# Kernel optimization log

Measured on AMD Instinct MI355X. Metric: run time of the kernel, lower is better.

The kernel has to match this reference:

```python
import jax, jax.numpy as jnp
import numpy as np

N_GRAPHS = 1000  # fixed num_segments (torch uses batch.max()+1; ids drawn in [0, N_GRAPHS))


def setup_inputs() -> dict:
    key = jax.random.key(0)
    ks = jax.random.split(key, 12)
    n, d, h, e = 100000, 128, 128, 1600000
    x = jax.random.normal(ks[0], (n, d), jnp.float32)
    edge_index = jax.random.randint(ks[1], (2, e), 0, n)
    batch = jnp.sort(jax.random.randint(ks[2], (n,), 0, N_GRAPHS))

    def lin_w(k, i, o):
        return jax.random.normal(k, (i, o), jnp.float32) / np.sqrt(i).astype(np.float32)

    return {
        "x": x, "edge_index": edge_index, "batch": batch,
        "W0": lin_w(ks[3], d, h), "b0": jnp.zeros((h,), jnp.float32),
        "W1": lin_w(ks[4], h, h), "b1": jnp.zeros((h,), jnp.float32),
        "W2": lin_w(ks[5], h, h), "b2": jnp.zeros((h,), jnp.float32),
        "Wp1": lin_w(ks[6], h, h), "bp1": jnp.zeros((h,), jnp.float32),
        "Wp2": lin_w(ks[7], h, 1), "bp2": jnp.zeros((1,), jnp.float32),
    }


def reference(x, edge_index, batch, W0, b0, W1, b1, W2, b2, Wp1, bp1, Wp2, bp2):
    n = x.shape[0]
    src, dst = edge_index[0], edge_index[1]
    loop = jnp.arange(n, dtype=edge_index.dtype)
    src_a = jnp.concatenate([src, loop])  # [E+N]
    dst_a = jnp.concatenate([dst, loop])  # [E+N]

    # degree with self-loops, symmetric GCN norm per edge
    deg = jax.ops.segment_sum(jnp.ones_like(dst_a, dtype=x.dtype), dst_a, num_segments=n)
    dd = deg[src_a] * deg[dst_a]
    norm = jnp.where(dd > 0, jax.lax.rsqrt(dd), jnp.zeros_like(dd))  # [E+N]

    for W, b in ((W0, b0), (W1, b1), (W2, b2)):
        h = x @ W + b                              # [N, H] dense linear
        msg = h[src_a] * norm[:, None]             # gather + scale, [E+N, H]
        out = jax.ops.segment_sum(msg, dst_a, num_segments=n)  # scatter-add
        x = jax.nn.relu(out)

    # segment-mean pool over graphs
    pool = jax.ops.segment_sum(x, batch, num_segments=N_GRAPHS)  # [G, H]
    cnt = jax.ops.segment_sum(jnp.ones((n,), x.dtype), batch, num_segments=N_GRAPHS)
    pool = pool / jnp.clip(cnt, 1.0)[:, None]

    hid = jax.nn.relu(pool @ Wp1 + bp1)
    return (hid @ Wp2 + bp2).squeeze(-1)  # [G]
```

## Files before the change

### kernel.cpp

```cpp
#include <hip/hip_runtime.h>
#include <hip/hip_bf16.h>
#include <math.h>


typedef float f32x4 __attribute__((ext_vector_type(4)));
typedef short s16x8 __attribute__((ext_vector_type(8)));
typedef _Float16 f16;
typedef _Float16 f16x4 __attribute__((ext_vector_type(4)));

__device__ __forceinline__ unsigned short f2bf(float x) {
  unsigned u = __float_as_uint(x);
  unsigned r = (u + 0x7FFFu + ((u >> 16) & 1u)) >> 16;
  return (unsigned short)r;
}

__device__ __forceinline__ void wsplit_body(
    int blk, const float* __restrict__ W0, const float* __restrict__ W1,
    const float* __restrict__ W2, short* __restrict__ Whi, short* __restrict__ Wlo) {
  int layer = blk >> 6;
  int i = (blk & 63) * 256 + threadIdx.x;
  const float* W = (layer == 0) ? W0 : (layer == 1) ? W1 : W2;
  int j = i & 7, lane = (i >> 3) & 63, ks = (i >> 9) & 3, nt = i >> 11;
  int k = ks * 32 + (lane >> 4) * 8 + j;
  int nn = nt * 16 + (lane & 15);
  float w = W[k * 128 + nn];
  unsigned short h = f2bf(w);
  float hf = __uint_as_float(((unsigned)h) << 16);
  Whi[layer * 16384 + i] = (short)h;
  Wlo[layer * 16384 + i] = (short)f2bf(w - hf);
}

__global__ __launch_bounds__(256) void uber0_kernel(
    const int* __restrict__ src, const int* __restrict__ dst,
    int* __restrict__ cnt, int* __restrict__ bucket, int E,
    const float* __restrict__ W0, const float* __restrict__ W1,
    const float* __restrict__ W2, short* __restrict__ Whi, short* __restrict__ Wlo,
    const int* __restrict__ batch, int* __restrict__ gptr, int n, int G,
    float* __restrict__ pool, int CD, int GBD) {
  int b = blockIdx.x;
  if (b < CD) {
    int e = b * 256 + threadIdx.x;
    if (e < E) {
      int s = src[e], d = dst[e];
      int r = atomicAdd(&cnt[d], 1);
      if (r < 64) bucket[(d << 6) + r] = s;
    }
  } else if (b < CD + 192) {
    wsplit_body(b - CD, W0, W1, W2, Whi, Wlo);
  } else if (b < CD + 192 + GBD) {
    int i = (b - CD - 192) * 256 + threadIdx.x;
    if (i < n) {
      int bb = batch[i];
      if (i == 0) {
        for (int g = 0; g <= bb; ++g) gptr[g] = 0;
      } else {
        int bp = batch[i - 1];
        for (int g = bp + 1; g <= bb; ++g) gptr[g] = i;
      }
      if (i == n - 1) {
        for (int g = bb + 1; g <= G; ++g) gptr[g] = n;
      }
    }
  } else {
    int i = (b - CD - 192 - GBD) * 256 + threadIdx.x;
    if (i * 4 < G * 128) ((float4*)pool)[i] = make_float4(0.f, 0.f, 0.f, 0.f);
  }
}

__global__ __launch_bounds__(256) void gemm1_kernel(
    const float* __restrict__ X, const short* __restrict__ Whi,
    const short* __restrict__ Wlo, const float* __restrict__ bias,
    const int* __restrict__ cnt, float* __restrict__ rsq,
    f16* __restrict__ H, int n) {
  int wave = threadIdx.x >> 6, lane = threadIdx.x & 63;
  int quad = lane >> 4, m = lane & 15;
  int mbase = blockIdx.x * 64 + wave * 16;
  int row = min(mbase + m, n - 1);
  const float* xr = X + (size_t)row * 128 + quad * 8;
  const s16x8* WH = (const s16x8*)Whi;
  const s16x8* WL = (const s16x8*)Wlo;
  f32x4 acc[8];
#pragma unroll
  for (int nt = 0; nt < 8; ++nt) acc[nt] = 0.f;
#pragma unroll
  for (int ks = 0; ks < 4; ++ks) {
    float4 xa = *(const float4*)(xr + ks * 32);
    float4 xb = *(const float4*)(xr + ks * 32 + 4);
    float xs[8] = {xa.x, xa.y, xa.z, xa.w, xb.x, xb.y, xb.z, xb.w};
    s16x8 ah, al;
#pragma unroll
    for (int j = 0; j < 8; ++j) {
      unsigned short h = f2bf(xs[j]);
      float hf = __uint_as_float(((unsigned)h) << 16);
      ah[j] = (short)h;
      al[j] = (short)f2bf(xs[j] - hf);
    }
#pragma unroll
    for (int nt = 0; nt < 8; ++nt) {
      s16x8 wh = WH[(nt * 4 + ks) * 64 + lane];
      s16x8 wl = WL[(nt * 4 + ks) * 64 + lane];
      acc[nt] = __builtin_amdgcn_mfma_f32_16x16x32_bf16(ah, wh, acc[nt], 0, 0, 0);
      acc[nt] = __builtin_amdgcn_mfma_f32_16x16x32_bf16(al, wh, acc[nt], 0, 0, 0);
      acc[nt] = __builtin_amdgcn_mfma_f32_16x16x32_bf16(ah, wl, acc[nt], 0, 0, 0);
    }
  }
  float rs[4];
#pragma unroll
  for (int r = 0; r < 4; ++r) {
    int rr = mbase + quad * 4 + r;
    rs[r] = (rr < n) ? (1.0f / sqrtf((float)(cnt[rr] + 1))) : 0.f;
  }
  if (m == 0) {
#pragma unroll
    for (int r = 0; r < 4; ++r) {
      int rr = mbase + quad * 4 + r;
      if (rr < n) rsq[rr] = rs[r];
    }
  }
#pragma unroll
  for (int nt = 0; nt < 8; ++nt) {
    int col = nt * 16 + m;
    float bb = bias[col];
#pragma unroll
    for (int r = 0; r < 4; ++r) {
      int rr = mbase + quad * 4 + r;
      if (rr < n) H[(size_t)rr * 128 + col] = (f16)((acc[nt][r] + bb) * rs[r]);
    }
  }
}

__device__ __forceinline__ f32x4 agg_sum(
    const f16* __restrict__ H, const int* __restrict__ cnt,
    const int* __restrict__ bucket, int node, int hl) {
  const char* Hb = (const char*)H;
  unsigned hoff = (unsigned)hl << 3;
  int beg = node << 6;
  int end = beg + min(cnt[node], 64);
  f32x4 a = __builtin_convertvector(
      *(const f16x4*)(Hb + (((unsigned)node << 8) | hoff)), f32x4);
#define ROW(s) (*(const f16x4*)(Hb + (((unsigned)(s) << 8) + hoff)))
  for (int base = beg; base < end; base += 32) {
    int m = end - base;
    if (m > 32) m = 32;
    int sl = (hl < m) ? bucket[base + hl] : 0;
    int j = 0;
    for (; j + 15 < m; j += 16) {
      int s0 = __shfl(sl, j + 0, 32), s1 = __shfl(sl, j + 1, 32);
      int s2 = __shfl(sl, j + 2, 32), s3 = __shfl(sl, j + 3, 32);
      int s4 = __shfl(sl, j + 4, 32), s5 = __shfl(sl, j + 5, 32);
      int s6 = __shfl(sl, j + 6, 32), s7 = __shfl(sl, j + 7, 32);
      int s8 = __shfl(sl, j + 8, 32), s9 = __shfl(sl, j + 9, 32);
      int sa = __shfl(sl, j + 10, 32), sb = __shfl(sl, j + 11, 32);
      int sc = __shfl(sl, j + 12, 32), sd = __shfl(sl, j + 13, 32);
      int se = __shfl(sl, j + 14, 32), sf = __shfl(sl, j + 15, 32);
      f16x4 h0 = ROW(s0), h1 = ROW(s1), h2 = ROW(s2), h3 = ROW(s3);
      f16x4 h4 = ROW(s4), h5 = ROW(s5), h6 = ROW(s6), h7 = ROW(s7);
      f16x4 h8 = ROW(s8), h9 = ROW(s9), ha = ROW(sa), hb = ROW(sb);
      f16x4 hc = ROW(sc), hd = ROW(sd), he = ROW(se), hf = ROW(sf);
      f16x4 t0 = ((h0 + h1) + (h2 + h3)) + ((h4 + h5) + (h6 + h7));
      f16x4 t1 = ((h8 + h9) + (ha + hb)) + ((hc + hd) + (he + hf));
      a += __builtin_convertvector(t0, f32x4);
      a += __builtin_convertvector(t1, f32x4);
    }
    for (; j + 7 < m; j += 8) {
      int s0 = __shfl(sl, j + 0, 32), s1 = __shfl(sl, j + 1, 32);
      int s2 = __shfl(sl, j + 2, 32), s3 = __shfl(sl, j + 3, 32);
      int s4 = __shfl(sl, j + 4, 32), s5 = __shfl(sl, j + 5, 32);
      int s6 = __shfl(sl, j + 6, 32), s7 = __shfl(sl, j + 7, 32);
      f16x4 h0 = ROW(s0), h1 = ROW(s1), h2 = ROW(s2), h3 = ROW(s3);
      f16x4 h4 = ROW(s4), h5 = ROW(s5), h6 = ROW(s6), h7 = ROW(s7);
      f16x4 t0 = ((h0 + h1) + (h2 + h3)) + ((h4 + h5) + (h6 + h7));
      a += __builtin_convertvector(t0, f32x4);
    }
    for (; j + 3 < m; j += 4) {
      int s0 = __shfl(sl, j + 0, 32), s1 = __shfl(sl, j + 1, 32);
      int s2 = __shfl(sl, j + 2, 32), s3 = __shfl(sl, j + 3, 32);
      f16x4 t0 = (ROW(s0) + ROW(s1)) + (ROW(s2) + ROW(s3));
      a += __builtin_convertvector(t0, f32x4);
    }
    for (; j < m; ++j) {
      int s0 = __shfl(sl, j, 32);
      a += __builtin_convertvector(ROW(s0), f32x4);
    }
  }
#undef ROW
  return a;
}

#define LDS_STRIDE 132
__global__ __launch_bounds__(256) void agg_gemm_kernel(
    const f16* __restrict__ H, const int* __restrict__ cnt,
    const int* __restrict__ bucket, const float* __restrict__ rsq,
    const short* __restrict__ Whi, const short* __restrict__ Wlo,
    const float* __restrict__ bias, f16* __restrict__ Hout, int n) {
  __shared__ int lds[16 * LDS_STRIDE];
  int hw = threadIdx.x >> 5, hl = threadIdx.x & 31;
  int nbase = blockIdx.x * 16;
#pragma unroll
  for (int rep = 0; rep < 2; ++rep) {
    int nl = hw + rep * 8;
    int node = nbase + nl;
    f32x4 o = 0.f;
    if (node < n) {
      f32x4 s = agg_sum(H, cnt, bucket, node, hl);
      float r = rsq[node];
      o.x = fmaxf(s.x * r, 0.f);
      o.y = fmaxf(s.y * r, 0.f);
      o.z = fmaxf(s.z * r, 0.f);
      o.w = fmaxf(s.w * r, 0.f);
    }
    int* dst = lds + nl * LDS_STRIDE + hl * 4;
#pragma unroll
    for (int c = 0; c < 4; ++c) {
      float v = o[c];
      unsigned short h = f2bf(v);
      float hf = __uint_as_float(((unsigned)h) << 16);
      unsigned short l = f2bf(v - hf);
      dst[c] = (int)((((unsigned)h) << 16) | l);
    }
  }
  __syncthreads();

  int wave = threadIdx.x >> 6, lane = threadIdx.x & 63;
  int quad = lane >> 4, m = lane & 15;
  const s16x8* WH = (const s16x8*)Whi;
  const s16x8* WL = (const s16x8*)Wlo;
  f32x4 acc0 = 0.f, acc1 = 0.f;
  int nt0 = wave * 2, nt1 = wave * 2 + 1;
#pragma unroll
  for (int ks = 0; ks < 4; ++ks) {
    const int* arow = lds + m * LDS_STRIDE + ks * 32 + quad * 8;
    s16x8 ah, al;
#pragma unroll
    for (int j = 0; j < 8; ++j) {
      unsigned p = (unsigned)arow[j];
      ah[j] = (short)(p >> 16);
      al[j] = (short)(p & 0xffffu);
    }
    s16x8 wh0 = WH[(nt0 * 4 + ks) * 64 + lane];
    s16x8 wl0 = WL[(nt0 * 4 + ks) * 64 + lane];
    s16x8 wh1 = WH[(nt1 * 4 + ks) * 64 + lane];
    s16x8 wl1 = WL[(nt1 * 4 + ks) * 64 + lane];
    acc0 = __builtin_amdgcn_mfma_f32_16x16x32_bf16(ah, wh0, acc0, 0, 0, 0);
    acc0 = __builtin_amdgcn_mfma_f32_16x16x32_bf16(al, wh0, acc0, 0, 0, 0);
    acc0 = __builtin_amdgcn_mfma_f32_16x16x32_bf16(ah, wl0, acc0, 0, 0, 0);
    acc1 = __builtin_amdgcn_mfma_f32_16x16x32_bf16(ah, wh1, acc1, 0, 0, 0);
    acc1 = __builtin_amdgcn_mfma_f32_16x16x32_bf16(al, wh1, acc1, 0, 0, 0);
    acc1 = __builtin_amdgcn_mfma_f32_16x16x32_bf16(ah, wl1, acc1, 0, 0, 0);
  }
  float rs[4];
#pragma unroll
  for (int r = 0; r < 4; ++r) {
    int rr = nbase + quad * 4 + r;
    rs[r] = (rr < n) ? rsq[rr] : 0.f;
  }
#pragma unroll
  for (int t = 0; t < 2; ++t) {
    int nt = wave * 2 + t;
    int col = nt * 16 + m;
    float b = bias[col];
    f32x4 a = t ? acc1 : acc0;
#pragma unroll
    for (int r = 0; r < 4; ++r) {
      int rr = nbase + quad * 4 + r;
      if (rr < n) Hout[(size_t)rr * 128 + col] = (f16)((a[r] + b) * rs[r]);
    }
  }
}

__global__ __launch_bounds__(256) void agg_pool_kernel(
    const f16* __restrict__ H, const int* __restrict__ cnt,
    const int* __restrict__ bucket, const float* __restrict__ rsq,
    const int* __restrict__ batch, float* __restrict__ pool, int n) {
  __shared__ float rows[16][128];
  __shared__ int gids[16];
  int hw = threadIdx.x >> 5, hl = threadIdx.x & 31;
  int nbase = blockIdx.x * 16;
#pragma unroll
  for (int rep = 0; rep < 2; ++rep) {
    int nl = hw + rep * 8;
    int node = nbase + nl;
    f32x4 o = 0.f;
    if (node < n) {
      f32x4 s = agg_sum(H, cnt, bucket, node, hl);
      float r = rsq[node];
      o.x = fmaxf(s.x * r, 0.f);
      o.y = fmaxf(s.y * r, 0.f);
      o.z = fmaxf(s.z * r, 0.f);
      o.w = fmaxf(s.w * r, 0.f);
    }
    *(f32x4*)&rows[nl][hl * 4] = o;
    if (hl == 0) gids[nl] = (node < n) ? batch[node] : -1;
  }
  __syncthreads();
  int half = threadIdx.x >> 7;
  int ch = threadIdx.x & 127;
  float acc = 0.f;
  int curg = gids[half * 8];
  for (int i = half * 8; i < half * 8 + 8; ++i) {
    int g = gids[i];
    if (g != curg) {
      if (curg >= 0) atomicAdd(&pool[(size_t)curg * 128 + ch], acc);
      acc = 0.f;
      curg = g;
    }
    if (g >= 0) acc += rows[i][ch];
  }
  if (curg >= 0) atomicAdd(&pool[(size_t)curg * 128 + ch], acc);
}

__global__ __launch_bounds__(128) void head_kernel(
    const float* __restrict__ pool, const int* __restrict__ gptr,
    const float* __restrict__ Wp1, const float* __restrict__ bp1,
    const float* __restrict__ Wp2, const float* __restrict__ bp2,
    float* __restrict__ out, int G) {
  int g = blockIdx.x;
  int j = threadIdx.x;
  __shared__ float ps[128];
  __shared__ float hs[128];
  int cnt = gptr[g + 1] - gptr[g];
  float inv = 1.0f / (float)max(cnt, 1);
  ps[j] = pool[(size_t)g * 128 + j] * inv;
  __syncthreads();
  float acc = bp1[j];
#pragma unroll 8
  for (int k = 0; k < 128; ++k) acc = fmaf(ps[k], Wp1[k * 128 + j], acc);
  hs[j] = fmaxf(acc, 0.f) * Wp2[j];
  __syncthreads();
  for (int off = 64; off > 0; off >>= 1) {
    if (j < off) hs[j] += hs[j + off];
    __syncthreads();
  }
  if (j == 0) out[g] = hs[0] + bp2[0];
}

extern "C" void kernel_launch(void* const* d_in, const int* in_sizes, int n_in,
                              void* d_out, int out_size, void* d_ws, size_t ws_size,
                              hipStream_t stream) {
  const float* x    = (const float*)d_in[0];
  const int*   eidx = (const int*)d_in[1];
  const int*   batch= (const int*)d_in[2];
  const float* W0 = (const float*)d_in[3];
  const float* b0 = (const float*)d_in[4];
  const float* W1 = (const float*)d_in[5];
  const float* b1 = (const float*)d_in[6];
  const float* W2 = (const float*)d_in[7];
  const float* b2 = (const float*)d_in[8];
  const float* Wp1 = (const float*)d_in[9];
  const float* bp1 = (const float*)d_in[10];
  const float* Wp2 = (const float*)d_in[11];
  const float* bp2 = (const float*)d_in[12];
  float* out = (float*)d_out;

  const int N = in_sizes[0] / 128;
  const int E = in_sizes[1] / 2;
  const int G = out_size;

  const int* src = eidx;
  const int* dst = eidx + E;

  char* ws = (char*)d_ws;
  size_t off = 0;
  auto alloc = [&](size_t bytes) -> void* {
    void* p = ws + off;
    off = (off + bytes + 255) & ~(size_t)255;
    return p;
  };
  int*   cnt     = (int*)  alloc((size_t)N * 4);
  int*   bucket  = (int*)  alloc((size_t)N * 64 * 4);
  float* rsq     = (float*)alloc((size_t)N * 4);
  f16*   bufA    = (f16*)  alloc((size_t)N * 128 * 2);
  f16*   bufB    = (f16*)  alloc((size_t)N * 128 * 2);
  int*   gptr    = (int*)  alloc((size_t)(G + 1) * 4);
  float* pool    = (float*)alloc((size_t)G * 128 * 4);
  short* whi     = (short*)alloc(3 * 16384 * 2);
  short* wlo     = (short*)alloc(3 * 16384 * 2);
  (void)ws_size;

  hipMemsetAsync(cnt, 0, (size_t)N * 4, stream);

  const int CD  = (E + 255) / 256;
  const int GBD = (N + 255) / 256;
  const int PZ  = (G * 128 / 4 + 255) / 256;
  uber0_kernel<<<CD + 192 + GBD + PZ, 256, 0, stream>>>(
      src, dst, cnt, bucket, E, W0, W1, W2, whi, wlo, batch, gptr, N, G, pool,
      CD, GBD);

  gemm1_kernel<<<(N + 63) / 64, 256, 0, stream>>>(
      x, whi, wlo, b0, cnt, rsq, bufA, N);

  dim3 fused_grid((N + 15) / 16);
  agg_gemm_kernel<<<fused_grid, 256, 0, stream>>>(bufA, cnt, bucket, rsq,
      whi + 16384, wlo + 16384, b1, bufB, N);
  agg_gemm_kernel<<<fused_grid, 256, 0, stream>>>(bufB, cnt, bucket, rsq,
      whi + 2 * 16384, wlo + 2 * 16384, b2, bufA, N);
  agg_pool_kernel<<<fused_grid, 256, 0, stream>>>(bufA, cnt, bucket, rsq, batch, pool, N);

  head_kernel<<<G, 128, 0, stream>>>(pool, gptr, Wp1, bp1, Wp2, bp2, out, G);
}
```

Baseline: 483.2 us.

## Tile feature buffers by channel group and split aggregation from GEMM

Stores layer activations as 8 column tiles of 16 fp16 channels each, contiguous per node. Aggregation is split into per-tile blocks so that the blockIdx&7 tile choice lines up with round-robin XCD dispatch, letting each XCD's L2 hold one roughly 3.2 MB tile during the random neighbour gathers. The fused agg+GEMM kernels are replaced by separate aggregation and full 128-wide GEMM kernels, which adds an intermediate buffer R that is written and read again. The edge bucket fill becomes a two-phase scheme: record per-edge ranks, then scatter with nontemporal stores inside the first GEMM launch. The degree normalization now clamps the neighbour count to 64.

```diff
diff --git a/kernel.cpp b/kernel.cpp
--- a/kernel.cpp
+++ b/kernel.cpp
@@ -7,6 +7,7 @@
 typedef short s16x8 __attribute__((ext_vector_type(8)));
 typedef _Float16 f16;
 typedef _Float16 f16x4 __attribute__((ext_vector_type(4)));
+typedef _Float16 f16x8 __attribute__((ext_vector_type(8)));
 
 __device__ __forceinline__ unsigned short f2bf(float x) {
   unsigned u = __float_as_uint(x);
@@ -31,8 +32,8 @@
 }
 
 __global__ __launch_bounds__(256) void uber0_kernel(
-    const int* __restrict__ src, const int* __restrict__ dst,
-    int* __restrict__ cnt, int* __restrict__ bucket, int E,
+    const int* __restrict__ dst, int* __restrict__ cnt, int* __restrict__ rank,
+    int E,
     const float* __restrict__ W0, const float* __restrict__ W1,
     const float* __restrict__ W2, short* __restrict__ Whi, short* __restrict__ Wlo,
     const int* __restrict__ batch, int* __restrict__ gptr, int n, int G,
@@ -41,9 +42,8 @@
   if (b < CD) {
     int e = b * 256 + threadIdx.x;
     if (e < E) {
-      int s = src[e], d = dst[e];
-      int r = atomicAdd(&cnt[d], 1);
-      if (r < 64) bucket[(d << 6) + r] = s;
+      int d = __builtin_nontemporal_load(dst + e);
+      rank[e] = atomicAdd(&cnt[d], 1);
     }
   } else if (b < CD + 192) {
     wsplit_body(b - CD, W0, W1, W2, Whi, Wlo);
@@ -67,14 +67,27 @@
   }
 }
 
-__global__ __launch_bounds__(256) void gemm1_kernel(
+__global__ __launch_bounds__(256) void fill_gemm1_kernel(
+    const int* __restrict__ src, const int* __restrict__ dstv,
+    const int* __restrict__ rank, int* __restrict__ bucket, int E, int FB,
     const float* __restrict__ X, const short* __restrict__ Whi,
     const short* __restrict__ Wlo, const float* __restrict__ bias,
-    const int* __restrict__ cnt, float* __restrict__ rsq,
-    f16* __restrict__ H, int n) {
+    const int* __restrict__ cnt, f16* __restrict__ H, int n) {
+  int b = blockIdx.x;
+  if (b < FB) {
+    int i = b * 256 + threadIdx.x;
+    if (i < E) {
+      int s = __builtin_nontemporal_load(src + i);
+      int d = __builtin_nontemporal_load(dstv + i);
+      int r = __builtin_nontemporal_load(rank + i);
+      if (r < 64)
+        __builtin_nontemporal_store(s, bucket + (((size_t)d) << 6) + r);
+    }
+    return;
+  }
   int wave = threadIdx.x >> 6, lane = threadIdx.x & 63;
   int quad = lane >> 4, m = lane & 15;
-  int mbase = blockIdx.x * 64 + wave * 16;
+  int mbase = (b - FB) * 64 + wave * 16;
   int row = min(mbase + m, n - 1);
   const float* xr = X + (size_t)row * 128 + quad * 8;
   const s16x8* WH = (const s16x8*)Whi;
@@ -108,14 +121,7 @@
 #pragma unroll
   for (int r = 0; r < 4; ++r) {
     int rr = mbase + quad * 4 + r;
-    rs[r] = (rr < n) ? (1.0f / sqrtf((float)(cnt[rr] + 1))) : 0.f;
-  }
-  if (m == 0) {
-#pragma unroll
-    for (int r = 0; r < 4; ++r) {
-      int rr = mbase + quad * 4 + r;
-      if (rr < n) rsq[rr] = rs[r];
-    }
+    rs[r] = (rr < n) ? (1.0f / sqrtf((float)(min(cnt[rr], 64) + 1))) : 0.f;
   }
 #pragma unroll
   for (int nt = 0; nt < 8; ++nt) {
@@ -124,189 +130,198 @@
 #pragma unroll
     for (int r = 0; r < 4; ++r) {
       int rr = mbase + quad * 4 + r;
-      if (rr < n) H[(size_t)rr * 128 + col] = (f16)((acc[nt][r] + bb) * rs[r]);
-    }
-  }
-}
-
-__device__ __forceinline__ f32x4 agg_sum(
-    const f16* __restrict__ H, const int* __restrict__ cnt,
-    const int* __restrict__ bucket, int node, int hl) {
-  const char* Hb = (const char*)H;
-  unsigned hoff = (unsigned)hl << 3;
-  int beg = node << 6;
-  int end = beg + min(cnt[node], 64);
-  f32x4 a = __builtin_convertvector(
-      *(const f16x4*)(Hb + (((unsigned)node << 8) | hoff)), f32x4);
-#define ROW(s) (*(const f16x4*)(Hb + (((unsigned)(s) << 8) + hoff)))
-  for (int base = beg; base < end; base += 32) {
-    int m = end - base;
-    if (m > 32) m = 32;
-    int sl = (hl < m) ? bucket[base + hl] : 0;
-    int j = 0;
-    for (; j + 15 < m; j += 16) {
-      int s0 = __shfl(sl, j + 0, 32), s1 = __shfl(sl, j + 1, 32);
-      int s2 = __shfl(sl, j + 2, 32), s3 = __shfl(sl, j + 3, 32);
-      int s4 = __shfl(sl, j + 4, 32), s5 = __shfl(sl, j + 5, 32);
-      int s6 = __shfl(sl, j + 6, 32), s7 = __shfl(sl, j + 7, 32);
-      int s8 = __shfl(sl, j + 8, 32), s9 = __shfl(sl, j + 9, 32);
-      int sa = __shfl(sl, j + 10, 32), sb = __shfl(sl, j + 11, 32);
-      int sc = __shfl(sl, j + 12, 32), sd = __shfl(sl, j + 13, 32);
-      int se = __shfl(sl, j + 14, 32), sf = __shfl(sl, j + 15, 32);
-      f16x4 h0 = ROW(s0), h1 = ROW(s1), h2 = ROW(s2), h3 = ROW(s3);
-      f16x4 h4 = ROW(s4), h5 = ROW(s5), h6 = ROW(s6), h7 = ROW(s7);
-      f16x4 h8 = ROW(s8), h9 = ROW(s9), ha = ROW(sa), hb = ROW(sb);
-      f16x4 hc = ROW(sc), hd = ROW(sd), he = ROW(se), hf = ROW(sf);
-      f16x4 t0 = ((h0 + h1) + (h2 + h3)) + ((h4 + h5) + (h6 + h7));
-      f16x4 t1 = ((h8 + h9) + (ha + hb)) + ((hc + hd) + (he + hf));
-      a += __builtin_convertvector(t0, f32x4);
-      a += __builtin_convertvector(t1, f32x4);
-    }
-    for (; j + 7 < m; j += 8) {
-      int s0 = __shfl(sl, j + 0, 32), s1 = __shfl(sl, j + 1, 32);
-      int s2 = __shfl(sl, j + 2, 32), s3 = __shfl(sl, j + 3, 32);
-      int s4 = __shfl(sl, j + 4, 32), s5 = __shfl(sl, j + 5, 32);
-      int s6 = __shfl(sl, j + 6, 32), s7 = __shfl(sl, j + 7, 32);
-      f16x4 h0 = ROW(s0), h1 = ROW(s1), h2 = ROW(s2), h3 = ROW(s3);
-      f16x4 h4 = ROW(s4), h5 = ROW(s5), h6 = ROW(s6), h7 = ROW(s7);
-      f16x4 t0 = ((h0 + h1) + (h2 + h3)) + ((h4 + h5) + (h6 + h7));
-      a += __builtin_convertvector(t0, f32x4);
-    }
-    for (; j + 3 < m; j += 4) {
-      int s0 = __shfl(sl, j + 0, 32), s1 = __shfl(sl, j + 1, 32);
-      int s2 = __shfl(sl, j + 2, 32), s3 = __shfl(sl, j + 3, 32);
-      f16x4 t0 = (ROW(s0) + ROW(s1)) + (ROW(s2) + ROW(s3));
-      a += __builtin_convertvector(t0, f32x4);
-    }
-    for (; j < m; ++j) {
-      int s0 = __shfl(sl, j, 32);
-      a += __builtin_convertvector(ROW(s0), f32x4);
-    }
-  }
-#undef ROW
+      if (rr < n) {
+        f16 v = (f16)((acc[nt][r] + bb) * rs[r]);
+        __builtin_nontemporal_store(v, H + ((size_t)nt * n + rr) * 16 + m);
+      }
+    }
+  }
+}
+
+__device__ __forceinline__ f32x4 tile_node_sum(
+    const char* Hb, const int* idxrow, int m, int g, int c4) {
+  f32x4 a = 0.f;
+  int j = g;
+  for (; j + 8 < m; j += 16) {
+    int s0 = idxrow[j], s1 = idxrow[j + 8];
+    f16x4 h0 = *(const f16x4*)(Hb + (((size_t)s0 << 5) + (c4 << 3)));
+    f16x4 h1 = *(const f16x4*)(Hb + (((size_t)s1 << 5) + (c4 << 3)));
+    a += __builtin_convertvector(h0, f32x4);
+    a += __builtin_convertvector(h1, f32x4);
+  }
+  for (; j < m; j += 8) {
+    int s0 = idxrow[j];
+    f16x4 h0 = *(const f16x4*)(Hb + (((size_t)s0 << 5) + (c4 << 3)));
+    a += __builtin_convertvector(h0, f32x4);
+  }
+#pragma unroll
+  for (int d = 4; d <= 16; d <<= 1) {
+    a.x += __shfl_xor(a.x, d);
+    a.y += __shfl_xor(a.y, d);
+    a.z += __shfl_xor(a.z, d);
+    a.w += __shfl_xor(a.w, d);
+  }
   return a;
 }
 
-#define LDS_STRIDE 132
-__global__ __launch_bounds__(256) void agg_gemm_kernel(
-    const f16* __restrict__ H, const int* __restrict__ cnt,
-    const int* __restrict__ bucket, const float* __restrict__ rsq,
-    const short* __restrict__ Whi, const short* __restrict__ Wlo,
-    const float* __restrict__ bias, f16* __restrict__ Hout, int n) {
-  __shared__ int lds[16 * LDS_STRIDE];
-  int hw = threadIdx.x >> 5, hl = threadIdx.x & 31;
-  int nbase = blockIdx.x * 16;
-#pragma unroll
-  for (int rep = 0; rep < 2; ++rep) {
-    int nl = hw + rep * 8;
+__global__ __launch_bounds__(256) void aggA_kernel(
+    const f16* __restrict__ Ht, const int* __restrict__ cnt,
+    const int* __restrict__ bucket, f16* __restrict__ Aout, int n) {
+  __shared__ int idx[64][65];
+  __shared__ int cnt_s[64];
+  int tid = threadIdx.x;
+  int tile = blockIdx.x & 7;
+  int nbase = (blockIdx.x >> 3) * 64;
+  if (tid < 64) {
+    int node = nbase + tid;
+    int c = (node < n) ? min(cnt[node], 64) : 0;
+    cnt_s[tid] = c + 1;
+    idx[tid][c] = (node < n) ? node : 0;
+  }
+  __syncthreads();
+  for (int i = tid; i < 64 * 64; i += 256) {
+    int nl = i >> 6, j = i & 63;
+    if (j < cnt_s[nl] - 1)
+      idx[nl][j] = __builtin_nontemporal_load(
+          bucket + (((size_t)(nbase + nl)) << 6) + j);
+  }
+  __syncthreads();
+  const char* Hb = (const char*)Ht + (((size_t)tile * n) << 5);
+  int hw = tid >> 5, hl = tid & 31, g = hl >> 2, c4 = hl & 3;
+  for (int rep = 0; rep < 8; ++rep) {
+    int nl = rep * 8 + hw;
     int node = nbase + nl;
-    f32x4 o = 0.f;
-    if (node < n) {
-      f32x4 s = agg_sum(H, cnt, bucket, node, hl);
-      float r = rsq[node];
-      o.x = fmaxf(s.x * r, 0.f);
-      o.y = fmaxf(s.y * r, 0.f);
-      o.z = fmaxf(s.z * r, 0.f);
-      o.w = fmaxf(s.w * r, 0.f);
-    }
-    int* dst = lds + nl * LDS_STRIDE + hl * 4;
-#pragma unroll
-    for (int c = 0; c < 4; ++c) {
-      float v = o[c];
-      unsigned short h = f2bf(v);
-      float hf = __uint_as_float(((unsigned)h) << 16);
-      unsigned short l = f2bf(v - hf);
-      dst[c] = (int)((((unsigned)h) << 16) | l);
-    }
-  }
-  __syncthreads();
-
+    if (node >= n) continue;
+    f32x4 a = tile_node_sum(Hb, idx[nl], cnt_s[nl], g, c4);
+    if (g == 0) {
+      float r = 1.0f / sqrtf((float)cnt_s[nl]);
+      f16x4 o;
+      o[0] = (f16)fmaxf(a.x * r, 0.f);
+      o[1] = (f16)fmaxf(a.y * r, 0.f);
+      o[2] = (f16)fmaxf(a.z * r, 0.f);
+      o[3] = (f16)fmaxf(a.w * r, 0.f);
+      __builtin_nontemporal_store(
+          o, (f16x4*)(Aout + ((size_t)node << 7) + (tile << 4) + (c4 << 2)));
+    }
+  }
+}
+
+__global__ __launch_bounds__(256) void aggA_pool_kernel(
+    const f16* __restrict__ Ht, const int* __restrict__ cnt,
+    const int* __restrict__ bucket, const int* __restrict__ batch,
+    float* __restrict__ pool, int n) {
+  __shared__ int idx[64][65];
+  __shared__ int cnt_s[64];
+  __shared__ float rows[64][16];
+  __shared__ int gids[64];
+  int tid = threadIdx.x;
+  int tile = blockIdx.x & 7;
+  int nbase = (blockIdx.x >> 3) * 64;
+  if (tid < 64) {
+    int node = nbase + tid;
+    int c = (node < n) ? min(cnt[node], 64) : 0;
+    cnt_s[tid] = c + 1;
+    idx[tid][c] = (node < n) ? node : 0;
+    gids[tid] = (node < n) ? batch[node] : -1;
+  }
+  __syncthreads();
+  for (int i = tid; i < 64 * 64; i += 256) {
+    int nl = i >> 6, j = i & 63;
+    if (j < cnt_s[nl] - 1)
+      idx[nl][j] = __builtin_nontemporal_load(
+          bucket + (((size_t)(nbase + nl)) << 6) + j);
+  }
+  __syncthreads();
+  const char* Hb = (const char*)Ht + (((size_t)tile * n) << 5);
+  int hw = tid >> 5, hl = tid & 31, g = hl >> 2, c4 = hl & 3;
+  for (int rep = 0; rep < 8; ++rep) {
+    int nl = rep * 8 + hw;
+    int node = nbase + nl;
+    f32x4 a = 0.f;
+    if (node < n) a = tile_node_sum(Hb, idx[nl], cnt_s[nl], g, c4);
+    if (g == 0) {
+      f32x4 o = 0.f;
+      if (node < n) {
+        float r = 1.0f / sqrtf((float)cnt_s[nl]);
+        o.x = fmaxf(a.x * r, 0.f);
+        o.y = fmaxf(a.y * r, 0.f);
+        o.z = fmaxf(a.z * r, 0.f);
+        o.w = fmaxf(a.w * r, 0.f);
+      }
+      *(f32x4*)&rows[nl][c4 << 2] = o;
+    }
+  }
+  __syncthreads();
+  if (tid < 16) {
+    int col = tid;
+    float acc = 0.f;
+    int curg = gids[0];
+    for (int i2 = 0; i2 < 64; ++i2) {
+      int gg = gids[i2];
+      if (gg != curg) {
+        if (curg >= 0) atomicAdd(&pool[(size_t)curg * 128 + (tile << 4) + col], acc);
+        acc = 0.f;
+        curg = gg;
+      }
+      if (gg >= 0) acc += rows[i2][col];
+    }
+    if (curg >= 0) atomicAdd(&pool[(size_t)curg * 128 + (tile << 4) + col], acc);
+  }
+}
+
+__global__ __launch_bounds__(256) void gemmB_kernel(
+    const f16* __restrict__ Ain, const short* __restrict__ Whi,
+    const short* __restrict__ Wlo, const float* __restrict__ bias,
+    const int* __restrict__ cnt, f16* __restrict__ Hout, int n) {
   int wave = threadIdx.x >> 6, lane = threadIdx.x & 63;
   int quad = lane >> 4, m = lane & 15;
+  int mbase = blockIdx.x * 64 + wave * 16;
+  int row = min(mbase + m, n - 1);
+  const f16* ar = Ain + (size_t)row * 128 + quad * 8;
   const s16x8* WH = (const s16x8*)Whi;
   const s16x8* WL = (const s16x8*)Wlo;
-  f32x4 acc0 = 0.f, acc1 = 0.f;
-  int nt0 = wave * 2, nt1 = wave * 2 + 1;
+  f32x4 acc[8];
+#pragma unroll
+  for (int nt = 0; nt < 8; ++nt) acc[nt] = 0.f;
 #pragma unroll
   for (int ks = 0; ks < 4; ++ks) {
-    const int* arow = lds + m * LDS_STRIDE + ks * 32 + quad * 8;
+    f16x8 v = __builtin_nontemporal_load((const f16x8*)(ar + ks * 32));
     s16x8 ah, al;
 #pragma unroll
     for (int j = 0; j < 8; ++j) {
-      unsigned p = (unsigned)arow[j];
-      ah[j] = (short)(p >> 16);
-      al[j] = (short)(p & 0xffffu);
-    }
-    s16x8 wh0 = WH[(nt0 * 4 + ks) * 64 + lane];
-    s16x8 wl0 = WL[(nt0 * 4 + ks) * 64 + lane];
-    s16x8 wh1 = WH[(nt1 * 4 + ks) * 64 + lane];
-    s16x8 wl1 = WL[(nt1 * 4 + ks) * 64 + lane];
-    acc0 = __builtin_amdgcn_mfma_f32_16x16x32_bf16(ah, wh0, acc0, 0, 0, 0);
-    acc0 = __builtin_amdgcn_mfma_f32_16x16x32_bf16(al, wh0, acc0, 0, 0, 0);
-    acc0 = __builtin_amdgcn_mfma_f32_16x16x32_bf16(ah, wl0, acc0, 0, 0, 0);
-    acc1 = __builtin_amdgcn_mfma_f32_16x16x32_bf16(ah, wh1, acc1, 0, 0, 0);
-    acc1 = __builtin_amdgcn_mfma_f32_16x16x32_bf16(al, wh1, acc1, 0, 0, 0);
-    acc1 = __builtin_amdgcn_mfma_f32_16x16x32_bf16(ah, wl1, acc1, 0, 0, 0);
+      float x = (float)v[j];
+      unsigned short h = f2bf(x);
+      float hf = __uint_as_float(((unsigned)h) << 16);
+      ah[j] = (short)h;
+      al[j] = (short)f2bf(x - hf);
+    }
+#pragma unroll
+    for (int nt = 0; nt < 8; ++nt) {
+      s16x8 wh = WH[(nt * 4 + ks) * 64 + lane];
+      s16x8 wl = WL[(nt * 4 + ks) * 64 + lane];
+      acc[nt] = __builtin_amdgcn_mfma_f32_16x16x32_bf16(ah, wh, acc[nt], 0, 0, 0);
+      acc[nt] = __builtin_amdgcn_mfma_f32_16x16x32_bf16(al, wh, acc[nt], 0, 0, 0);
+      acc[nt] = __builtin_amdgcn_mfma_f32_16x16x32_bf16(ah, wl, acc[nt], 0, 0, 0);
+    }
   }
   float rs[4];
 #pragma unroll
   for (int r = 0; r < 4; ++r) {
-    int rr = nbase + quad * 4 + r;
-    rs[r] = (rr < n) ? rsq[rr] : 0.f;
-  }
-#pragma unroll
-  for (int t = 0; t < 2; ++t) {
-    int nt = wave * 2 + t;
-    int col = nt * 16 + m;
-    float b = bias[col];
-    f32x4 a = t ? acc1 : acc0;
+    int rr = mbase + quad * 4 + r;
+    rs[r] = (rr < n) ? (1.0f / sqrtf((float)(min(cnt[rr], 64) + 1))) : 0.f;
+  }
+#pragma unroll
+  for (int nt = 0; nt < 8; ++nt) {
+    float bb = bias[nt * 16 + m];
 #pragma unroll
     for (int r = 0; r < 4; ++r) {
-      int rr = nbase + quad * 4 + r;
-      if (rr < n) Hout[(size_t)rr * 128 + col] = (f16)((a[r] + b) * rs[r]);
-    }
-  }
-}
-
-__global__ __launch_bounds__(256) void agg_pool_kernel(
-    const f16* __restrict__ H, const int* __restrict__ cnt,
-    const int* __restrict__ bucket, const float* __restrict__ rsq,
-    const int* __restrict__ batch, float* __restrict__ pool, int n) {
-  __shared__ float rows[16][128];
-  __shared__ int gids[16];
-  int hw = threadIdx.x >> 5, hl = threadIdx.x & 31;
-  int nbase = blockIdx.x * 16;
-#pragma unroll
-  for (int rep = 0; rep < 2; ++rep) {
-    int nl = hw + rep * 8;
-    int node = nbase + nl;
-    f32x4 o = 0.f;
-    if (node < n) {
-      f32x4 s = agg_sum(H, cnt, bucket, node, hl);
-      float r = rsq[node];
-      o.x = fmaxf(s.x * r, 0.f);
-      o.y = fmaxf(s.y * r, 0.f);
-      o.z = fmaxf(s.z * r, 0.f);
-      o.w = fmaxf(s.w * r, 0.f);
-    }
-    *(f32x4*)&rows[nl][hl * 4] = o;
-    if (hl == 0) gids[nl] = (node < n) ? batch[node] : -1;
-  }
-  __syncthreads();
-  int half = threadIdx.x >> 7;
-  int ch = threadIdx.x & 127;
-  float acc = 0.f;
-  int curg = gids[half * 8];
-  for (int i = half * 8; i < half * 8 + 8; ++i) {
-    int g = gids[i];
-    if (g != curg) {
-      if (curg >= 0) atomicAdd(&pool[(size_t)curg * 128 + ch], acc);
-      acc = 0.f;
-      curg = g;
-    }
-    if (g >= 0) acc += rows[i][ch];
-  }
-  if (curg >= 0) atomicAdd(&pool[(size_t)curg * 128 + ch], acc);
+      int rr = mbase + quad * 4 + r;
+      if (rr < n) {
+        f16 v = (f16)((acc[nt][r] + bb) * rs[r]);
+        __builtin_nontemporal_store(v, Hout + ((size_t)nt * n + rr) * 16 + m);
+      }
+    }
+  }
 }
 
 __global__ __launch_bounds__(128) void head_kernel(
@@ -367,10 +382,11 @@
     return p;
   };
   int*   cnt     = (int*)  alloc((size_t)N * 4);
+  int*   rank    = (int*)  alloc((size_t)E * 4);
   int*   bucket  = (int*)  alloc((size_t)N * 64 * 4);
-  float* rsq     = (float*)alloc((size_t)N * 4);
-  f16*   bufA    = (f16*)  alloc((size_t)N * 128 * 2);
-  f16*   bufB    = (f16*)  alloc((size_t)N * 128 * 2);
+  f16*   T0      = (f16*)  alloc((size_t)N * 128 * 2);
+  f16*   T1      = (f16*)  alloc((size_t)N * 128 * 2);
+  f16*   R       = (f16*)  alloc((size_t)N * 128 * 2);
   int*   gptr    = (int*)  alloc((size_t)(G + 1) * 4);
   float* pool    = (float*)alloc((size_t)G * 128 * 4);
   short* whi     = (short*)alloc(3 * 16384 * 2);
@@ -383,18 +399,22 @@
   const int GBD = (N + 255) / 256;
   const int PZ  = (G * 128 / 4 + 255) / 256;
   uber0_kernel<<<CD + 192 + GBD + PZ, 256, 0, stream>>>(
-      src, dst, cnt, bucket, E, W0, W1, W2, whi, wlo, batch, gptr, N, G, pool,
+      dst, cnt, rank, E, W0, W1, W2, whi, wlo, batch, gptr, N, G, pool,
       CD, GBD);
 
-  gemm1_kernel<<<(N + 63) / 64, 256, 0, stream>>>(
-      x, whi, wlo, b0, cnt, rsq, bufA, N);
-
-  dim3 fused_grid((N + 15) / 16);
-  agg_gemm_kernel<<<fused_grid, 256, 0, stream>>>(bufA, cnt, bucket, rsq,
-      whi + 16384, wlo + 16384, b1, bufB, N);
-  agg_gemm_kernel<<<fused_grid, 256, 0, stream>>>(bufB, cnt, bucket, rsq,
-      whi + 2 * 16384, wlo + 2 * 16384, b2, bufA, N);
-  agg_pool_kernel<<<fused_grid, 256, 0, stream>>>(bufA, cnt, bucket, rsq, batch, pool, N);
+  const int FB  = (E + 255) / 256;
+  const int GB1 = (N + 63) / 64;
+  fill_gemm1_kernel<<<FB + GB1, 256, 0, stream>>>(
+      src, dst, rank, bucket, E, FB, x, whi, wlo, b0, cnt, T0, N);
+
+  const int NB = (N + 63) / 64;
+  aggA_kernel<<<8 * NB, 256, 0, stream>>>(T0, cnt, bucket, R, N);
+  gemmB_kernel<<<GB1, 256, 0, stream>>>(R, whi + 16384, wlo + 16384, b1,
+                                        cnt, T1, N);
+  aggA_kernel<<<8 * NB, 256, 0, stream>>>(T1, cnt, bucket, R, N);
+  gemmB_kernel<<<GB1, 256, 0, stream>>>(R, whi + 2 * 16384, wlo + 2 * 16384,
+                                        b2, cnt, T0, N);
+  aggA_pool_kernel<<<8 * NB, 256, 0, stream>>>(T0, cnt, bucket, batch, pool, N);
 
   head_kernel<<<G, 128, 0, stream>>>(pool, gptr, Wp1, bp1, Wp2, bp2, out, G);
 }
```

Result: slower. 876.2 us (+81.3%).

## Split edge bucketing into rank atomics and deferred fill fused with first GEMM

Applied to the files above, without the earlier changes.

The counting pass now only does the atomic increment per edge and stores its rank. Writing the source into the bucket moves into a new fused kernel whose leading blocks scatter the bucket entries while later blocks run the first-layer GEMM. The aim is to take the dependent bucket store out of the atomic pass and overlap the scatter with GEMM work. In exchange it adds an E-sized rank array that is written once and read back, plus a second read of src and dst.

```diff
diff --git a/kernel.cpp b/kernel.cpp
--- a/kernel.cpp
+++ b/kernel.cpp
@@ -31,8 +31,8 @@
 }
 
 __global__ __launch_bounds__(256) void uber0_kernel(
-    const int* __restrict__ src, const int* __restrict__ dst,
-    int* __restrict__ cnt, int* __restrict__ bucket, int E,
+    const int* __restrict__ dst, int* __restrict__ cnt, int* __restrict__ rank,
+    int E,
     const float* __restrict__ W0, const float* __restrict__ W1,
     const float* __restrict__ W2, short* __restrict__ Whi, short* __restrict__ Wlo,
     const int* __restrict__ batch, int* __restrict__ gptr, int n, int G,
@@ -40,11 +40,7 @@
   int b = blockIdx.x;
   if (b < CD) {
     int e = b * 256 + threadIdx.x;
-    if (e < E) {
-      int s = src[e], d = dst[e];
-      int r = atomicAdd(&cnt[d], 1);
-      if (r < 64) bucket[(d << 6) + r] = s;
-    }
+    if (e < E) rank[e] = atomicAdd(&cnt[dst[e]], 1);
   } else if (b < CD + 192) {
     wsplit_body(b - CD, W0, W1, W2, Whi, Wlo);
   } else if (b < CD + 192 + GBD) {
@@ -67,14 +63,25 @@
   }
 }
 
-__global__ __launch_bounds__(256) void gemm1_kernel(
+__global__ __launch_bounds__(256) void fill_gemm1_kernel(
+    const int* __restrict__ src, const int* __restrict__ dstv,
+    const int* __restrict__ rank, int* __restrict__ bucket, int E, int FB,
     const float* __restrict__ X, const short* __restrict__ Whi,
     const short* __restrict__ Wlo, const float* __restrict__ bias,
     const int* __restrict__ cnt, float* __restrict__ rsq,
     f16* __restrict__ H, int n) {
+  int b = blockIdx.x;
+  if (b < FB) {
+    int i = b * 256 + threadIdx.x;
+    if (i < E) {
+      int s = src[i], d = dstv[i], r = rank[i];
+      if (r < 64) bucket[(((size_t)d) << 6) + r] = s;
+    }
+    return;
+  }
   int wave = threadIdx.x >> 6, lane = threadIdx.x & 63;
   int quad = lane >> 4, m = lane & 15;
-  int mbase = blockIdx.x * 64 + wave * 16;
+  int mbase = (b - FB) * 64 + wave * 16;
   int row = min(mbase + m, n - 1);
   const float* xr = X + (size_t)row * 128 + quad * 8;
   const s16x8* WH = (const s16x8*)Whi;
@@ -367,6 +374,7 @@
     return p;
   };
   int*   cnt     = (int*)  alloc((size_t)N * 4);
+  int*   rank    = (int*)  alloc((size_t)E * 4);
   int*   bucket  = (int*)  alloc((size_t)N * 64 * 4);
   float* rsq     = (float*)alloc((size_t)N * 4);
   f16*   bufA    = (f16*)  alloc((size_t)N * 128 * 2);
@@ -383,11 +391,13 @@
   const int GBD = (N + 255) / 256;
   const int PZ  = (G * 128 / 4 + 255) / 256;
   uber0_kernel<<<CD + 192 + GBD + PZ, 256, 0, stream>>>(
-      src, dst, cnt, bucket, E, W0, W1, W2, whi, wlo, batch, gptr, N, G, pool,
+      dst, cnt, rank, E, W0, W1, W2, whi, wlo, batch, gptr, N, G, pool,
       CD, GBD);
 
-  gemm1_kernel<<<(N + 63) / 64, 256, 0, stream>>>(
-      x, whi, wlo, b0, cnt, rsq, bufA, N);
+  const int FB = (E + 255) / 256;
+  const int GB = (N + 63) / 64;
+  fill_gemm1_kernel<<<FB + GB, 256, 0, stream>>>(
+      src, dst, rank, bucket, E, FB, x, whi, wlo, b0, cnt, rsq, bufA, N);
 
   dim3 fused_grid((N + 15) / 16);
   agg_gemm_kernel<<<fused_grid, 256, 0, stream>>>(bufA, cnt, bucket, rsq,
```

New measurement: 449.0 us. 1.08x faster.
